# Performance work log

Measured on AMD Instinct MI355X. Metric: run time of the kernel, lower is better.

Reference implementation:

```python
import jax, jax.numpy as jnp
import numpy as np

WS = 10      # window_size
HID = 32     # hidden_dim
B, T = 1024, 4096


def setup_inputs() -> dict:
    key = jax.random.key(0)
    k = jax.random.split(key, 7)
    returns = jax.random.normal(k[0], (B, T), dtype=jnp.float32) * 0.01
    W1 = jax.random.normal(k[1], (WS, HID), dtype=jnp.float32) * (1.0 / np.sqrt(WS))
    b1 = jnp.zeros((HID,), dtype=jnp.float32)
    W2 = jax.random.normal(k[2], (HID, HID), dtype=jnp.float32) * (1.0 / np.sqrt(HID))
    b2 = jnp.zeros((HID,), dtype=jnp.float32)
    W3 = jax.random.normal(k[3], (HID, 1), dtype=jnp.float32) * (1.0 / np.sqrt(HID))
    b3 = jnp.zeros((1,), dtype=jnp.float32)
    return {"returns": returns, "W1": W1, "b1": b1, "W2": W2, "b2": b2, "W3": W3, "b3": b3}


def reference(returns, W1, b1, W2, b2, W3, b3):
    ws = W1.shape[0]
    Bb, Tt = returns.shape
    # Unfold all sliding windows at once: windows[b, i, :] = returns[b, i:i+ws]
    # (window ending just before timestep t = i + ws)
    idx = jnp.arange(Tt - ws)[:, None] + jnp.arange(ws)[None, :]  # [T-ws, ws]
    windows = returns[:, idx]                                     # [B, T-ws, ws]
    h = jax.nn.relu(windows @ W1 + b1)                            # [B, T-ws, HID]
    h = jax.nn.relu(h @ W2 + b2)                                  # [B, T-ws, HID]
    out = 0.5 * jax.nn.sigmoid((h @ W3 + b3).squeeze(-1))         # [B, T-ws]
    # H_local[:, t] = out[:, t-ws] for t >= ws; first ws columns copy column ws
    head = jnp.broadcast_to(out[:, :1], (Bb, ws))                 # [B, ws]
    return jnp.concatenate([head, out], axis=1)                   # [B, T]
```

## Files before the change

kernel.cpp:

```cpp
#include <hip/hip_runtime.h>
#include <math.h>

typedef _Float16 f16x8  __attribute__((ext_vector_type(8)));
typedef _Float16 h2v    __attribute__((ext_vector_type(2)));
typedef float    f32x16 __attribute__((ext_vector_type(16)));
typedef float    f32x4  __attribute__((ext_vector_type(4)));
typedef __fp16   h2a    __attribute__((ext_vector_type(2)));
typedef unsigned u32x4  __attribute__((ext_vector_type(4)));

#define WS    10
#define HID   32
#define BDIM  256
#define NWAVE 4
#define GN    32
#define T_LEN 4096
#define NGRP  (T_LEN / GN)

__device__ inline unsigned pack2u(float a, float b) {
    h2a t = __builtin_amdgcn_cvt_pkrtz(a, b);
    return __builtin_bit_cast(unsigned, t);
}
__device__ inline unsigned relu2(unsigned u) {
    h2v x = __builtin_bit_cast(h2v, u);
    h2v z = {(_Float16)0.0f, (_Float16)0.0f};
    return __builtin_bit_cast(unsigned, __builtin_elementwise_max(x, z));
}

__device__ inline void load_win(const float* __restrict__ rptr, int t, int hi,
                                float e2[2], float v6[6]) {
    const int ws = (t >= WS) ? (t - WS) : 0;
    __builtin_memcpy(e2, &rptr[ws + 8 * hi], 8);
    __builtin_memcpy(v6, &rptr[ws + 2], 24);
}

__global__ __launch_bounds__(BDIM, 2)
void hurst_ilp2v(const float* __restrict__ returns,
                 const float* __restrict__ W1, const float* __restrict__ b1,
                 const float* __restrict__ W2, const float* __restrict__ b2,
                 const float* __restrict__ W3, const float* __restrict__ b3,
                 float* __restrict__ out)
{
    const int tid  = threadIdx.x;
    const int wid  = tid >> 6;
    const int lane = tid & 63;
    const int n    = lane & 31;
    const int hi   = lane >> 5;

    f32x16 b1v, b2v;
    #pragma unroll
    for (int i = 0; i < 4; ++i) {
        const f32x4 v1 = ((const f32x4*)b1)[2 * i + hi];
        const f32x4 v2 = ((const f32x4*)b2)[2 * i + hi];
        #pragma unroll
        for (int o = 0; o < 4; ++o) {
            b1v[4 * i + o] = v1[o];
            b2v[4 * i + o] = v2[o];
        }
    }
    const float corr = b3[0] - b2[4 * hi];

    f16x8 a1, a2lo, a2hi, a3lo, a3hi;
    #pragma unroll
    for (int jj = 0; jj < 8; ++jj) {
        const int k  = 8 * hi + jj;
        a1[jj] = (k < WS) ? (_Float16)W1[k * HID + n] : (_Float16)0.0f;
        const int kf = (k & 3) | ((k & 4) << 1) | ((k & 8) >> 1);
        a2lo[jj] = (_Float16)W2[kf * HID + n];
        a2hi[jj] = (_Float16)W2[(16 + kf) * HID + n];
        a3lo[jj] = (_Float16)W3[kf];
        a3hi[jj] = (_Float16)W3[16 + kf];
    }

    const float* rptr = returns + (size_t)blockIdx.x * T_LEN;
    float*       optr = out     + (size_t)blockIdx.x * T_LEN;

    float e2c[2][2], v6c[2][6];
    load_win(rptr, wid * GN + n,           hi, e2c[0], v6c[0]);
    load_win(rptr, (wid + NWAVE) * GN + n, hi, e2c[1], v6c[1]);

    for (int g = wid; g < NGRP; g += 2 * NWAVE) {
        const int gp = (g + 2 * NWAVE < NGRP) ? (g + 2 * NWAVE) : g;
        float e2n[2][2], v6n[2][6];
        load_win(rptr, gp * GN + n,           hi, e2n[0], v6n[0]);
        load_win(rptr, (gp + NWAVE) * GN + n, hi, e2n[1], v6n[1]);

        f16x8 xb[2];
        #pragma unroll
        for (int c = 0; c < 2; ++c) {
            u32x4 xu;
            xu[0] = pack2u(e2c[c][0], e2c[c][1]);
            xu[1] = hi ? 0u : pack2u(v6c[c][0], v6c[c][1]);
            xu[2] = hi ? 0u : pack2u(v6c[c][2], v6c[c][3]);
            xu[3] = hi ? 0u : pack2u(v6c[c][4], v6c[c][5]);
            xb[c] = __builtin_bit_cast(f16x8, xu);
        }

        f32x16 d1[2];
        #pragma unroll
        for (int c = 0; c < 2; ++c)
            d1[c] = __builtin_amdgcn_mfma_f32_32x32x16_f16(a1, xb[c], b1v, 0, 0, 0);

        u32x4 p1lo[2], p1hi[2];
        #pragma unroll
        for (int c = 0; c < 2; ++c)
            #pragma unroll
            for (int i = 0; i < 4; ++i) {
                p1lo[c][i] = relu2(pack2u(d1[c][2 * i],     d1[c][2 * i + 1]));
                p1hi[c][i] = relu2(pack2u(d1[c][8 + 2 * i], d1[c][9 + 2 * i]));
            }

        f32x16 d2[2];
        #pragma unroll
        for (int c = 0; c < 2; ++c)
            d2[c] = __builtin_amdgcn_mfma_f32_32x32x16_f16(
                        a2lo, __builtin_bit_cast(f16x8, p1lo[c]), b2v, 0, 0, 0);
        #pragma unroll
        for (int c = 0; c < 2; ++c)
            d2[c] = __builtin_amdgcn_mfma_f32_32x32x16_f16(
                        a2hi, __builtin_bit_cast(f16x8, p1hi[c]), d2[c], 0, 0, 0);

        u32x4 p2lo[2], p2hi[2];
        #pragma unroll
        for (int c = 0; c < 2; ++c)
            #pragma unroll
            for (int i = 0; i < 4; ++i) {
                p2lo[c][i] = relu2(pack2u(d2[c][2 * i],     d2[c][2 * i + 1]));
                p2hi[c][i] = relu2(pack2u(d2[c][8 + 2 * i], d2[c][9 + 2 * i]));
            }

        f32x16 d3[2];
        #pragma unroll
        for (int c = 0; c < 2; ++c)
            d3[c] = __builtin_amdgcn_mfma_f32_32x32x16_f16(
                        a3lo, __builtin_bit_cast(f16x8, p2lo[c]), b2v, 0, 0, 0);
        #pragma unroll
        for (int c = 0; c < 2; ++c)
            d3[c] = __builtin_amdgcn_mfma_f32_32x32x16_f16(
                        a3hi, __builtin_bit_cast(f16x8, p2hi[c]), d3[c], 0, 0, 0);

        float o[2];
        #pragma unroll
        for (int c = 0; c < 2; ++c)
            o[c] = 0.5f * __builtin_amdgcn_rcpf(1.0f + __expf(-(d3[c][0] + corr)));

        if (hi == 0) {
            optr[g * GN + n]           = o[0];
            optr[(g + NWAVE) * GN + n] = o[1];
        }

        #pragma unroll
        for (int c = 0; c < 2; ++c) {
            #pragma unroll
            for (int i = 0; i < 2; ++i) e2c[c][i] = e2n[c][i];
            #pragma unroll
            for (int i = 0; i < 6; ++i) v6c[c][i] = v6n[c][i];
        }
    }
}

extern "C" void kernel_launch(void* const* d_in, const int* in_sizes, int n_in,
                              void* d_out, int out_size, void* d_ws, size_t ws_size,
                              hipStream_t stream) {
    const float* returns = (const float*)d_in[0];
    const float* W1      = (const float*)d_in[1];
    const float* b1      = (const float*)d_in[2];
    const float* W2      = (const float*)d_in[3];
    const float* b2      = (const float*)d_in[4];
    const float* W3      = (const float*)d_in[5];
    const float* b3      = (const float*)d_in[6];
    float* out = (float*)d_out;

    const int B = out_size / T_LEN;

    dim3 grid(B, 1, 1);
    dim3 block(BDIM, 1, 1);
    hurst_ilp2v<<<grid, block, 0, stream>>>(returns, W1, b1, W2, b2, W3, b3, out);
}
```

Before: 101.1 us.

## Process two batch rows per block with four independent MFMA chains per iteration

Each block now handles two rows of the batch, and each iteration works on four window groups instead of two, which gives more independent MFMA chains for latency hiding. The explicit software prefetch of the next iteration's windows is dropped in favour of loading inside the loop. The grid shrinks to B/2 blocks. This lowers the block count and raises register pressure, which could reduce occupancy, and removing the prefetch may expose load latency.

```diff
diff --git a/kernel.cpp b/kernel.cpp
--- a/kernel.cpp
+++ b/kernel.cpp
@@ -15,6 +15,7 @@
 #define GN    32
 #define T_LEN 4096
 #define NGRP  (T_LEN / GN)
+#define NIT   16
 
 __device__ inline unsigned pack2u(float a, float b) {
     h2a t = __builtin_amdgcn_cvt_pkrtz(a, b);
@@ -26,19 +27,12 @@
     return __builtin_bit_cast(unsigned, __builtin_elementwise_max(x, z));
 }
 
-__device__ inline void load_win(const float* __restrict__ rptr, int t, int hi,
-                                float e2[2], float v6[6]) {
-    const int ws = (t >= WS) ? (t - WS) : 0;
-    __builtin_memcpy(e2, &rptr[ws + 8 * hi], 8);
-    __builtin_memcpy(v6, &rptr[ws + 2], 24);
-}
-
 __global__ __launch_bounds__(BDIM, 2)
-void hurst_ilp2v(const float* __restrict__ returns,
-                 const float* __restrict__ W1, const float* __restrict__ b1,
-                 const float* __restrict__ W2, const float* __restrict__ b2,
-                 const float* __restrict__ W3, const float* __restrict__ b3,
-                 float* __restrict__ out)
+void hurst_ilp4(const float* __restrict__ returns,
+                const float* __restrict__ W1, const float* __restrict__ b1,
+                const float* __restrict__ W2, const float* __restrict__ b2,
+                const float* __restrict__ W3, const float* __restrict__ b3,
+                float* __restrict__ out)
 {
     const int tid  = threadIdx.x;
     const int wid  = tid >> 6;
@@ -71,89 +65,89 @@
         a3hi[jj] = (_Float16)W3[16 + kf];
     }
 
-    const float* rptr = returns + (size_t)blockIdx.x * T_LEN;
-    float*       optr = out     + (size_t)blockIdx.x * T_LEN;
+    const float* rA = returns + (size_t)(2 * blockIdx.x) * T_LEN;
+    const float* rB = rA + T_LEN;
+    float*       oA = out + (size_t)(2 * blockIdx.x) * T_LEN;
+    float*       oB = oA + T_LEN;
 
-    float e2c[2][2], v6c[2][6];
-    load_win(rptr, wid * GN + n,           hi, e2c[0], v6c[0]);
-    load_win(rptr, (wid + NWAVE) * GN + n, hi, e2c[1], v6c[1]);
+    for (int i = 0; i < NIT; ++i) {
+        const int g1  = wid + 8 * i;
+        const int g2  = g1 + 4;
+        const int t1  = g1 * GN + n;
+        const int t2  = g2 * GN + n;
+        const int ws1 = (t1 >= WS) ? (t1 - WS) : 0;
+        const int ws2 = (t2 >= WS) ? (t2 - WS) : 0;
 
-    for (int g = wid; g < NGRP; g += 2 * NWAVE) {
-        const int gp = (g + 2 * NWAVE < NGRP) ? (g + 2 * NWAVE) : g;
-        float e2n[2][2], v6n[2][6];
-        load_win(rptr, gp * GN + n,           hi, e2n[0], v6n[0]);
-        load_win(rptr, (gp + NWAVE) * GN + n, hi, e2n[1], v6n[1]);
+        float e2[4][2], v6[4][6];
+        __builtin_memcpy(e2[0], rA + ws1 + 8 * hi, 8);  __builtin_memcpy(v6[0], rA + ws1 + 2, 24);
+        __builtin_memcpy(e2[1], rB + ws1 + 8 * hi, 8);  __builtin_memcpy(v6[1], rB + ws1 + 2, 24);
+        __builtin_memcpy(e2[2], rA + ws2 + 8 * hi, 8);  __builtin_memcpy(v6[2], rA + ws2 + 2, 24);
+        __builtin_memcpy(e2[3], rB + ws2 + 8 * hi, 8);  __builtin_memcpy(v6[3], rB + ws2 + 2, 24);
 
-        f16x8 xb[2];
+        f16x8 xb[4];
         #pragma unroll
-        for (int c = 0; c < 2; ++c) {
+        for (int c = 0; c < 4; ++c) {
             u32x4 xu;
-            xu[0] = pack2u(e2c[c][0], e2c[c][1]);
-            xu[1] = hi ? 0u : pack2u(v6c[c][0], v6c[c][1]);
-            xu[2] = hi ? 0u : pack2u(v6c[c][2], v6c[c][3]);
-            xu[3] = hi ? 0u : pack2u(v6c[c][4], v6c[c][5]);
+            xu[0] = pack2u(e2[c][0], e2[c][1]);
+            xu[1] = hi ? 0u : pack2u(v6[c][0], v6[c][1]);
+            xu[2] = hi ? 0u : pack2u(v6[c][2], v6[c][3]);
+            xu[3] = hi ? 0u : pack2u(v6[c][4], v6[c][5]);
             xb[c] = __builtin_bit_cast(f16x8, xu);
         }
 
-        f32x16 d1[2];
+        f32x16 d1[4];
         #pragma unroll
-        for (int c = 0; c < 2; ++c)
+        for (int c = 0; c < 4; ++c)
             d1[c] = __builtin_amdgcn_mfma_f32_32x32x16_f16(a1, xb[c], b1v, 0, 0, 0);
 
-        u32x4 p1lo[2], p1hi[2];
+        u32x4 p1lo[4], p1hi[4];
         #pragma unroll
-        for (int c = 0; c < 2; ++c)
+        for (int c = 0; c < 4; ++c)
             #pragma unroll
-            for (int i = 0; i < 4; ++i) {
-                p1lo[c][i] = relu2(pack2u(d1[c][2 * i],     d1[c][2 * i + 1]));
-                p1hi[c][i] = relu2(pack2u(d1[c][8 + 2 * i], d1[c][9 + 2 * i]));
+            for (int q = 0; q < 4; ++q) {
+                p1lo[c][q] = relu2(pack2u(d1[c][2 * q],     d1[c][2 * q + 1]));
+                p1hi[c][q] = relu2(pack2u(d1[c][8 + 2 * q], d1[c][9 + 2 * q]));
             }
 
-        f32x16 d2[2];
+        f32x16 d2[4];
         #pragma unroll
-        for (int c = 0; c < 2; ++c)
+        for (int c = 0; c < 4; ++c)
             d2[c] = __builtin_amdgcn_mfma_f32_32x32x16_f16(
                         a2lo, __builtin_bit_cast(f16x8, p1lo[c]), b2v, 0, 0, 0);
         #pragma unroll
-        for (int c = 0; c < 2; ++c)
+        for (int c = 0; c < 4; ++c)
             d2[c] = __builtin_amdgcn_mfma_f32_32x32x16_f16(
                         a2hi, __builtin_bit_cast(f16x8, p1hi[c]), d2[c], 0, 0, 0);
 
-        u32x4 p2lo[2], p2hi[2];
+        u32x4 p2lo[4], p2hi[4];
         #pragma unroll
-        for (int c = 0; c < 2; ++c)
+        for (int c = 0; c < 4; ++c)
             #pragma unroll
-            for (int i = 0; i < 4; ++i) {
-                p2lo[c][i] = relu2(pack2u(d2[c][2 * i],     d2[c][2 * i + 1]));
-                p2hi[c][i] = relu2(pack2u(d2[c][8 + 2 * i], d2[c][9 + 2 * i]));
+            for (int q = 0; q < 4; ++q) {
+                p2lo[c][q] = relu2(pack2u(d2[c][2 * q],     d2[c][2 * q + 1]));
+                p2hi[c][q] = relu2(pack2u(d2[c][8 + 2 * q], d2[c][9 + 2 * q]));
             }
 
-        f32x16 d3[2];
+        f32x16 d3[4];
         #pragma unroll
-        for (int c = 0; c < 2; ++c)
+        for (int c = 0; c < 4; ++c)
             d3[c] = __builtin_amdgcn_mfma_f32_32x32x16_f16(
                         a3lo, __builtin_bit_cast(f16x8, p2lo[c]), b2v, 0, 0, 0);
         #pragma unroll
-        for (int c = 0; c < 2; ++c)
+        for (int c = 0; c < 4; ++c)
             d3[c] = __builtin_amdgcn_mfma_f32_32x32x16_f16(
                         a3hi, __builtin_bit_cast(f16x8, p2hi[c]), d3[c], 0, 0, 0);
 
-        float o[2];
+        float o[4];
         #pragma unroll
-        for (int c = 0; c < 2; ++c)
+        for (int c = 0; c < 4; ++c)
             o[c] = 0.5f * __builtin_amdgcn_rcpf(1.0f + __expf(-(d3[c][0] + corr)));
 
         if (hi == 0) {
-            optr[g * GN + n]           = o[0];
-            optr[(g + NWAVE) * GN + n] = o[1];
-        }
-
-        #pragma unroll
-        for (int c = 0; c < 2; ++c) {
-            #pragma unroll
-            for (int i = 0; i < 2; ++i) e2c[c][i] = e2n[c][i];
-            #pragma unroll
-            for (int i = 0; i < 6; ++i) v6c[c][i] = v6n[c][i];
+            oA[t1] = o[0];
+            oB[t1] = o[1];
+            oA[t2] = o[2];
+            oB[t2] = o[3];
         }
     }
 }
@@ -172,7 +166,7 @@
 
     const int B = out_size / T_LEN;
 
-    dim3 grid(B, 1, 1);
+    dim3 grid(B / 2, 1, 1);
     dim3 block(BDIM, 1, 1);
-    hurst_ilp2v<<<grid, block, 0, stream>>>(returns, W1, b1, W2, b2, W3, b3, out);
+    hurst_ilp4<<<grid, block, 0, stream>>>(returns, W1, b1, W2, b2, W3, b3, out);
 }
```

Result: faster. 98.67 us (-2.4%).
